# Kernel optimization log

Measured on AMD Instinct MI355X. Metric: run time of the kernel, lower is better.

Reference implementation:

```python
import jax, jax.numpy as jnp
import numpy as np

N = 100000      # nodes
E = 1600000     # edges (avg degree 16)
D_IN, D_H, D_OUT = 128, 128, 40
BN_EPS = 1e-5


def _gcn_norm(edge_index):
    # add self-loops, compute symmetric normalization D^-1/2 (A+I) D^-1/2
    loops = jnp.arange(N, dtype=edge_index.dtype)
    src = jnp.concatenate([edge_index[0], loops])
    dst = jnp.concatenate([edge_index[1], loops])
    deg = jax.ops.segment_sum(jnp.ones(src.shape[0], jnp.float32), dst, num_segments=N)
    dinv = jnp.where(deg > 0, jax.lax.rsqrt(deg), 0.0)
    norm = dinv[src] * dinv[dst]  # [E+N]
    return src, dst, norm


def _gcn_conv(h, W, b, src, dst, norm):
    h = h @ W                          # [N, d_out]
    msg = h[src] * norm[:, None]       # [E+N, d_out] gather + scale
    out = jax.ops.segment_sum(msg, dst, num_segments=N)
    return out + b


def _bn(h, g, beta, mean, var):
    return g * (h - mean) * jax.lax.rsqrt(var + BN_EPS) + beta


def setup_inputs() -> dict:
    key = jax.random.key(0)
    ks = jax.random.split(key, 16)
    x = jax.random.normal(ks[0], (N, D_IN), jnp.float32)
    edge_index = jax.random.randint(ks[1], (2, E), 0, N, dtype=jnp.int32)
    s_in, s_h = 1.0 / np.sqrt(D_IN), 1.0 / np.sqrt(D_H)
    W0 = jax.random.normal(ks[2], (D_IN, D_H), jnp.float32) * s_in
    b0 = jnp.zeros((D_H,), jnp.float32)
    W1 = jax.random.normal(ks[3], (D_H, D_H), jnp.float32) * s_h
    b1 = jnp.zeros((D_H,), jnp.float32)
    W2 = jax.random.normal(ks[4], (D_H, D_OUT), jnp.float32) * s_h
    b2 = jnp.zeros((D_OUT,), jnp.float32)
    g0 = jnp.ones((D_H,), jnp.float32)
    be0 = jnp.zeros((D_H,), jnp.float32)
    m0 = jax.random.normal(ks[5], (D_H,), jnp.float32) * 0.1
    v0 = jax.random.uniform(ks[6], (D_H,), jnp.float32) + 0.5
    g1 = jnp.ones((D_H,), jnp.float32)
    be1 = jnp.zeros((D_H,), jnp.float32)
    m1 = jax.random.normal(ks[7], (D_H,), jnp.float32) * 0.1
    v1 = jax.random.uniform(ks[8], (D_H,), jnp.float32) + 0.5
    return {"x": x, "edge_index": edge_index,
            "W0": W0, "b0": b0, "W1": W1, "b1": b1, "W2": W2, "b2": b2,
            "g0": g0, "be0": be0, "m0": m0, "v0": v0,
            "g1": g1, "be1": be1, "m1": m1, "v1": v1}


def reference(x, edge_index, W0, b0, W1, b1, W2, b2,
              g0, be0, m0, v0, g1, be1, m1, v1):
    src, dst, norm = _gcn_norm(edge_index)
    h = _gcn_conv(x, W0, b0, src, dst, norm)
    h = jax.nn.relu(_bn(h, g0, be0, m0, v0))   # dropout = identity in eval
    h = _gcn_conv(h, W1, b1, src, dst, norm)
    h = jax.nn.relu(_bn(h, g1, be1, m1, v1))
    h = _gcn_conv(h, W2, b2, src, dst, norm)
    return jax.nn.log_softmax(h, axis=1)
```

## Files before the change

### kernel.cpp

```cpp
#include <hip/hip_runtime.h>
#include <math.h>


#define CSHIFT 9
#define CSZ 512
#define PCHUNK 4096

typedef unsigned short u16;
typedef unsigned int u32;
typedef unsigned char u8;
typedef float f32x4 __attribute__((ext_vector_type(4)));
typedef short s16x8 __attribute__((ext_vector_type(8)));

__device__ inline float bflo(u32 u) { return __uint_as_float(u << 16); }
__device__ inline float bfhi(u32 u) { return __uint_as_float(u & 0xffff0000u); }
__device__ inline u16 f2bf(float f) {
    u32 b = __float_as_uint(f);
    b += 0x7fff + ((b >> 16) & 1);
    return (u16)(b >> 16);
}
__device__ inline u32 pack2(float lo, float hi) {
    return (u32)f2bf(lo) | ((u32)f2bf(hi) << 16);
}


__global__ __launch_bounds__(256) void k_hist1(const int* __restrict__ dst,
                                               int* __restrict__ hist1,
                                               int E, int NB) {
    __shared__ int h[256];
    int t = threadIdx.x;
    h[t] = 0;
    __syncthreads();
    for (int i = blockIdx.x * 256 * 16 + t; i < min(E, (blockIdx.x + 1) * 256 * 16);
         i += 256)
        atomicAdd(&h[dst[i] >> CSHIFT], 1);
    __syncthreads();
    if (t < NB && h[t]) atomicAdd(&hist1[t], h[t]);
}

__global__ __launch_bounds__(256) void k_scan1(const int* __restrict__ hist1,
                                               int* __restrict__ base1,
                                               int* __restrict__ cur1,
                                               int NB, int E) {
    __shared__ int sc[256];
    int t = threadIdx.x;
    int v = (t < NB) ? hist1[t] : 0;
    sc[t] = v;
    __syncthreads();
    for (int d = 1; d < 256; d <<= 1) {
        int add = (t >= d) ? sc[t - d] : 0;
        __syncthreads();
        sc[t] += add;
        __syncthreads();
    }
    if (t < NB) {
        int excl = sc[t] - v;
        base1[t] = excl;
        cur1[t] = excl;
    }
    if (t == 0) base1[NB] = E;
}

__global__ __launch_bounds__(256) void k_part1(const int* __restrict__ src,
                                               const int* __restrict__ dst,
                                               int* __restrict__ cur1,
                                               u32* __restrict__ bkt,
                                               int E, int NB) {
    __shared__ u32 stage[PCHUNK];
    __shared__ u8 sbin[PCHUNK];
    __shared__ int cnt[256];
    __shared__ int lbase[256];
    __shared__ int lcur[256];
    __shared__ int gb[256];
    int t = threadIdx.x;
    int base = blockIdx.x * PCHUNK;
    int n = min(PCHUNK, E - base);
    cnt[t] = 0;
    __syncthreads();
    for (int i = t; i < n; i += 256) atomicAdd(&cnt[dst[base + i] >> CSHIFT], 1);
    __syncthreads();
    int v = cnt[t];
    lbase[t] = v;
    __syncthreads();
    for (int d = 1; d < 256; d <<= 1) {
        int add = (t >= d) ? lbase[t - d] : 0;
        __syncthreads();
        lbase[t] += add;
        __syncthreads();
    }
    {
        int excl = lbase[t] - v;
        __syncthreads();
        lbase[t] = excl;
        lcur[t] = excl;
        if (t < NB && v) gb[t] = atomicAdd(&cur1[t], v);
    }
    __syncthreads();
    for (int i = t; i < n; i += 256) {
        int d = dst[base + i];
        int s = src[base + i];
        int bin = d >> CSHIFT;
        int p = atomicAdd(&lcur[bin], 1);
        stage[p] = ((u32)s << CSHIFT) | (u32)(d & (CSZ - 1));
        sbin[p] = (u8)bin;
    }
    __syncthreads();
    for (int k = t; k < n; k += 256) {
        int bin = sbin[k];
        bkt[gb[bin] + (k - lbase[bin])] = stage[k];
    }
}

__global__ __launch_bounds__(1024) void k_csr(const u32* __restrict__ bkt,
                                              const int* __restrict__ base1,
                                              int* __restrict__ col,
                                              int* __restrict__ row,
                                              float* __restrict__ dinv,
                                              int N, int E) {
    __shared__ int deg[CSZ];
    __shared__ int cur[CSZ];
    int b = blockIdx.x;
    int t = threadIdx.x;
    int start = base1[b];
    int end = base1[b + 1];
    if (t < CSZ) deg[t] = 0;
    __syncthreads();
    for (int i = start + t; i < end; i += 1024)
        atomicAdd(&deg[bkt[i] & (CSZ - 1)], 1);
    __syncthreads();
    int v = (t < CSZ) ? deg[t] : 0;
    if (t < CSZ) cur[t] = v;
    __syncthreads();
    for (int d = 1; d < CSZ; d <<= 1) {
        int add = (t < CSZ && t >= d) ? cur[t - d] : 0;
        __syncthreads();
        if (t < CSZ) cur[t] += add;
        __syncthreads();
    }
    if (t < CSZ) {
        int excl = cur[t] - v;
        int node = (b << CSHIFT) + t;
        if (node < N) {
            row[node] = start + excl;
            dinv[node] = rsqrtf((float)(v + 1));
        }
        cur[t] = excl;
    }
    __syncthreads();
    for (int i = start + t; i < end; i += 1024) {
        u32 e = bkt[i];
        int p = start + atomicAdd(&cur[e & (CSZ - 1)], 1);
        col[p] = (int)(e >> CSHIFT);
    }
    if (b == 0 && t == 0) row[N] = E;
}


__global__ __launch_bounds__(256) void k_packW(const float* __restrict__ W,
                                               u16* __restrict__ Wpk) {
    int g = blockIdx.x * 256 + threadIdx.x;
    int j = g & 7;
    int l = (g >> 3) & 63;
    int f = g >> 9;
    int ct = f & 7, ks = f >> 3;
    int krow = ks * 32 + ((l >> 4) << 3) + j;
    int wcol = ct * 16 + (l & 15);
    Wpk[g] = f2bf(W[krow * 128 + wcol]);
}

__global__ __launch_bounds__(256) void k_packW40(const float* __restrict__ W,
                                                 u16* __restrict__ Wpk) {
    int g = blockIdx.x * 256 + threadIdx.x;
    if (g >= 12 * 512) return;
    int j = g & 7;
    int l = (g >> 3) & 63;
    int f = g >> 9;
    int ct = f % 3, ks = f / 3;
    int krow = ks * 32 + ((l >> 4) << 3) + j;
    int wcol = ct * 16 + (l & 15);
    Wpk[g] = (wcol < 40) ? f2bf(W[krow * 40 + wcol]) : (u16)0;
}


__global__ __launch_bounds__(256) void k_gemm0(const float* __restrict__ A,
                                               const u16* __restrict__ Wpk,
                                               u16* __restrict__ C,
                                               const float* __restrict__ dinv,
                                               int M) {
    int tid = threadIdx.x;
    int wv = blockIdx.x * 4 + (tid >> 6);
    int rowbase = wv * 16;
    if (rowbase >= M) return;
    int l = tid & 63;
    int r = l & 15, hi = l >> 4;

    f32x4 acc[8];
#pragma unroll
    for (int ct = 0; ct < 8; ++ct) acc[ct] = (f32x4)(0.f);

    const uint4* wp = (const uint4*)Wpk;
#pragma unroll
    for (int ks = 0; ks < 4; ++ks) {
        int abase = (min(rowbase + r, M - 1)) * 128 + ks * 32 + hi * 8;
        float4 a0 = *(const float4*)&A[abase];
        float4 a1 = *(const float4*)&A[abase + 4];
        uint4 u = make_uint4(pack2(a0.x, a0.y), pack2(a0.z, a0.w),
                             pack2(a1.x, a1.y), pack2(a1.z, a1.w));
        s16x8 afrag = *(s16x8*)&u;
#pragma unroll
        for (int ct = 0; ct < 8; ++ct) {
            uint4 b = wp[(ks * 8 + ct) * 64 + l];
            s16x8 bfrag = *(s16x8*)&b;
            acc[ct] = __builtin_amdgcn_mfma_f32_16x16x32_bf16(afrag, bfrag, acc[ct], 0, 0, 0);
        }
    }
#pragma unroll
    for (int ct = 0; ct < 8; ++ct) {
#pragma unroll
        for (int reg = 0; reg < 4; ++reg) {
            int orow = rowbase + 4 * hi + reg;
            if (orow < M)
                C[(size_t)orow * 128 + ct * 16 + r] = f2bf(dinv[orow] * acc[ct][reg]);
        }
    }
}


template <int NCT>
__global__ __launch_bounds__(256) void k_fused(const u16* __restrict__ X,
                                               const u16* __restrict__ Wpk,
                                               u16* __restrict__ O,
                                               const int* __restrict__ row,
                                               const int* __restrict__ col,
                                               const float* __restrict__ dinv,
                                               const float* __restrict__ bias,
                                               const float* __restrict__ g,
                                               const float* __restrict__ be,
                                               const float* __restrict__ mean,
                                               const float* __restrict__ var,
                                               int n, int ostride) {
    __shared__ u32 hl[4][2][64];
    int tid = threadIdx.x;
    int wid = tid >> 6, lane = tid & 63;
    int half = lane >> 5, l5 = lane & 31;
    int node = (blockIdx.x * 4 + wid) * 2 + half;
    int nc = min(node, n - 1);
    const uint2* xp = (const uint2*)X;
    int s = row[nc], e = row[nc + 1];

    uint2 v = xp[(size_t)nc * 32 + l5];
    float a0 = bflo(v.x), a1 = bfhi(v.x), a2 = bflo(v.y), a3 = bfhi(v.y);
    float b0 = 0, b1 = 0, b2 = 0, b3 = 0;
    float c0 = 0, c1 = 0, c2 = 0, c3 = 0;
    float d0 = 0, d1 = 0, d2 = 0, d3 = 0;
    int j = s;
    for (; j + 8 <= e; j += 8) {
        int e0 = col[j], e1 = col[j+1], e2 = col[j+2], e3 = col[j+3];
        int e4 = col[j+4], e5 = col[j+5], e6 = col[j+6], e7 = col[j+7];
        uint2 x0 = xp[(size_t)e0 * 32 + l5];
        uint2 x1 = xp[(size_t)e1 * 32 + l5];
        uint2 x2 = xp[(size_t)e2 * 32 + l5];
        uint2 x3 = xp[(size_t)e3 * 32 + l5];
        uint2 x4 = xp[(size_t)e4 * 32 + l5];
        uint2 x5 = xp[(size_t)e5 * 32 + l5];
        uint2 x6 = xp[(size_t)e6 * 32 + l5];
        uint2 x7 = xp[(size_t)e7 * 32 + l5];
        a0 += bflo(x0.x); a1 += bfhi(x0.x); a2 += bflo(x0.y); a3 += bfhi(x0.y);
        b0 += bflo(x1.x); b1 += bfhi(x1.x); b2 += bflo(x1.y); b3 += bfhi(x1.y);
        c0 += bflo(x2.x); c1 += bfhi(x2.x); c2 += bflo(x2.y); c3 += bfhi(x2.y);
        d0 += bflo(x3.x); d1 += bfhi(x3.x); d2 += bflo(x3.y); d3 += bfhi(x3.y);
        a0 += bflo(x4.x); a1 += bfhi(x4.x); a2 += bflo(x4.y); a3 += bfhi(x4.y);
        b0 += bflo(x5.x); b1 += bfhi(x5.x); b2 += bflo(x5.y); b3 += bfhi(x5.y);
        c0 += bflo(x6.x); c1 += bfhi(x6.x); c2 += bflo(x6.y); c3 += bfhi(x6.y);
        d0 += bflo(x7.x); d1 += bfhi(x7.x); d2 += bflo(x7.y); d3 += bfhi(x7.y);
    }
    for (; j + 2 <= e; j += 2) {
        int e0 = col[j], e1 = col[j+1];
        uint2 x0 = xp[(size_t)e0 * 32 + l5];
        uint2 x1 = xp[(size_t)e1 * 32 + l5];
        a0 += bflo(x0.x); a1 += bfhi(x0.x); a2 += bflo(x0.y); a3 += bfhi(x0.y);
        b0 += bflo(x1.x); b1 += bfhi(x1.x); b2 += bflo(x1.y); b3 += bfhi(x1.y);
    }
    if (j < e) {
        uint2 x0 = xp[(size_t)col[j] * 32 + l5];
        c0 += bflo(x0.x); c1 += bfhi(x0.x); c2 += bflo(x0.y); c3 += bfhi(x0.y);
    }
    float dvn = dinv[nc];
    float s0 = dvn * ((a0 + b0) + (c0 + d0));
    float s1 = dvn * ((a1 + b1) + (c1 + d1));
    float s2 = dvn * ((a2 + b2) + (c2 + d2));
    float s3 = dvn * ((a3 + b3) + (c3 + d3));
    float4 g4 = ((const float4*)g)[l5];
    float4 be4 = ((const float4*)be)[l5];
    float4 m4 = ((const float4*)mean)[l5];
    float4 v4 = ((const float4*)var)[l5];
    float4 bi4 = ((const float4*)bias)[l5];
    float sc0 = g4.x * rsqrtf(v4.x + 1e-5f);
    float sc1 = g4.y * rsqrtf(v4.y + 1e-5f);
    float sc2 = g4.z * rsqrtf(v4.z + 1e-5f);
    float sc3 = g4.w * rsqrtf(v4.w + 1e-5f);
    float y0 = fmaxf(fmaf(sc0, s0, fmaf(sc0, bi4.x - m4.x, be4.x)), 0.f);
    float y1 = fmaxf(fmaf(sc1, s1, fmaf(sc1, bi4.y - m4.y, be4.y)), 0.f);
    float y2 = fmaxf(fmaf(sc2, s2, fmaf(sc2, bi4.z - m4.z, be4.z)), 0.f);
    float y3 = fmaxf(fmaf(sc3, s3, fmaf(sc3, bi4.w - m4.w, be4.w)), 0.f);

    *(uint2*)&hl[wid][half][l5 * 2] = make_uint2(pack2(y0, y1), pack2(y2, y3));

    int l = lane;
    int r1 = l & 1, hi = l >> 4;
    int node0 = (blockIdx.x * 4 + wid) * 2;
    int node1 = node0 + 1;
    float dv0 = dinv[min(node0, n - 1)];
    float dv1 = dinv[min(node1, n - 1)];
    const uint4* wp = (const uint4*)Wpk;
    const u32* hw = &hl[wid][0][0];
#pragma unroll
    for (int ct = 0; ct < NCT; ++ct) {
        f32x4 acc = (f32x4)(0.f);
#pragma unroll
        for (int ks = 0; ks < 4; ++ks) {
            uint4 a = *(const uint4*)&hw[r1 * 64 + ks * 16 + hi * 4];
            s16x8 afrag = *(s16x8*)&a;
            uint4 b = wp[(ks * NCT + ct) * 64 + l];
            s16x8 bfrag = *(s16x8*)&b;
            acc = __builtin_amdgcn_mfma_f32_16x16x32_bf16(afrag, bfrag, acc, 0, 0, 0);
        }
        if (l < 16) {
            int oc = ct * 16 + l;
            if (NCT == 8 || oc < 40) {
                if (node0 < n) O[(size_t)node0 * ostride + oc] = f2bf(dv0 * acc[0]);
                if (node1 < n) O[(size_t)node1 * ostride + oc] = f2bf(dv1 * acc[1]);
            }
        }
    }
}


__global__ __launch_bounds__(256) void k_agg40(const u16* __restrict__ X,
                                               float* __restrict__ out,
                                               const int* __restrict__ row,
                                               const int* __restrict__ col,
                                               const float* __restrict__ dinv,
                                               const float* __restrict__ b2,
                                               int n) {
    int tid = threadIdx.x;
    int wid = tid >> 6, lane = tid & 63;
    int half = lane >> 5, l5 = lane & 31;
    int node = (blockIdx.x * 4 + wid) * 2 + half;
    bool valid = node < n;
    int nc = valid ? node : (n - 1);
    bool active = l5 < 20;
    const u32* xp = (const u32*)X;
    int s = row[nc], e = row[nc + 1];
    int li = min(l5, 19);
    float a0 = 0, a1 = 0, b0 = 0, b1 = 0, c0 = 0, c1 = 0, d0 = 0, d1 = 0;
    {
        u32 v = xp[(size_t)nc * 20 + li];
        a0 = bflo(v); a1 = bfhi(v);
    }
    int j = s;
    for (; j + 8 <= e; j += 8) {
        int e0 = col[j], e1 = col[j+1], e2 = col[j+2], e3 = col[j+3];
        int e4 = col[j+4], e5 = col[j+5], e6 = col[j+6], e7 = col[j+7];
        u32 x0 = xp[(size_t)e0 * 20 + li];
        u32 x1 = xp[(size_t)e1 * 20 + li];
        u32 x2 = xp[(size_t)e2 * 20 + li];
        u32 x3 = xp[(size_t)e3 * 20 + li];
        u32 x4 = xp[(size_t)e4 * 20 + li];
        u32 x5 = xp[(size_t)e5 * 20 + li];
        u32 x6 = xp[(size_t)e6 * 20 + li];
        u32 x7 = xp[(size_t)e7 * 20 + li];
        a0 += bflo(x0); a1 += bfhi(x0);
        b0 += bflo(x1); b1 += bfhi(x1);
        c0 += bflo(x2); c1 += bfhi(x2);
        d0 += bflo(x3); d1 += bfhi(x3);
        a0 += bflo(x4); a1 += bfhi(x4);
        b0 += bflo(x5); b1 += bfhi(x5);
        c0 += bflo(x6); c1 += bfhi(x6);
        d0 += bflo(x7); d1 += bfhi(x7);
    }
    for (; j + 2 <= e; j += 2) {
        int e0 = col[j], e1 = col[j+1];
        u32 x0 = xp[(size_t)e0 * 20 + li];
        u32 x1 = xp[(size_t)e1 * 20 + li];
        a0 += bflo(x0); a1 += bfhi(x0);
        b0 += bflo(x1); b1 += bfhi(x1);
    }
    if (j < e) {
        u32 x0 = xp[(size_t)col[j] * 20 + li];
        c0 += bflo(x0); c1 += bfhi(x0);
    }
    float dv = dinv[nc];
    float ylo = -INFINITY, yhi = -INFINITY;
    if (active) {
        float2 bb = ((const float2*)b2)[l5];
        ylo = fmaf(dv, (a0 + b0) + (c0 + d0), bb.x);
        yhi = fmaf(dv, (a1 + b1) + (c1 + d1), bb.y);
    }
    float m = fmaxf(ylo, yhi);
#pragma unroll
    for (int d = 16; d; d >>= 1) m = fmaxf(m, __shfl_xor(m, d));
    float ex = active ? (__expf(ylo - m) + __expf(yhi - m)) : 0.f;
#pragma unroll
    for (int d = 16; d; d >>= 1) ex += __shfl_xor(ex, d);
    if (valid && active) {
        float lse = m + __logf(ex);
        ((float2*)out)[(size_t)node * 20 + l5] = make_float2(ylo - lse, yhi - lse);
    }
}


extern "C" void kernel_launch(void* const* d_in, const int* in_sizes, int n_in,
                              void* d_out, int out_size, void* d_ws, size_t ws_size,
                              hipStream_t stream) {
    const float* x   = (const float*)d_in[0];
    const int*   ei  = (const int*)d_in[1];
    const float* W0  = (const float*)d_in[2];
    const float* b0  = (const float*)d_in[3];
    const float* W1  = (const float*)d_in[4];
    const float* b1  = (const float*)d_in[5];
    const float* W2  = (const float*)d_in[6];
    const float* b2  = (const float*)d_in[7];
    const float* g0  = (const float*)d_in[8];
    const float* be0 = (const float*)d_in[9];
    const float* m0  = (const float*)d_in[10];
    const float* v0  = (const float*)d_in[11];
    const float* g1  = (const float*)d_in[12];
    const float* be1 = (const float*)d_in[13];
    const float* m1  = (const float*)d_in[14];
    const float* v1  = (const float*)d_in[15];
    float* out = (float*)d_out;

    int N = in_sizes[0] / 128;
    int E = in_sizes[1] / 2;
    const int* src = ei;
    const int* dst = ei + E;

    int NB = (N + CSZ - 1) / CSZ;

    char* ws = (char*)d_ws;
    size_t off = 0;
    auto alloc = [&](size_t bytes) -> char* {
        char* p = ws + off;
        off += (bytes + 255) & ~(size_t)255;
        return p;
    };
    u16*   XsA   = (u16*)alloc((size_t)N * 128 * 2);
    u16*   XsB   = (u16*)alloc((size_t)N * 128 * 2);
    u16*   bufC  = (u16*)alloc((size_t)N * 40 * 2);
    int*   col   = (int*)alloc((size_t)E * 4 + 64);
    int*   row   = (int*)alloc((size_t)(N + 1) * 4);
    float* dinv  = (float*)alloc((size_t)N * 4);
    int*   hist1 = (int*)alloc((size_t)(NB + 1) * 4);
    int*   base1 = (int*)alloc((size_t)(NB + 1) * 4);
    int*   cur1  = (int*)alloc((size_t)(NB + 1) * 4);
    u16*   Wpk0  = (u16*)alloc(128 * 128 * 2);
    u16*   Wpk1  = (u16*)alloc(128 * 128 * 2);
    u16*   Wpk2  = (u16*)alloc(128 * 48 * 2);
    u32*   bkt   = (u32*)XsA;

    hipMemsetAsync(hist1, 0, (size_t)(NB + 1) * 4, stream);
    k_hist1<<<(E + 4095) / 4096, 256, 0, stream>>>(dst, hist1, E, NB);
    k_scan1<<<1, 256, 0, stream>>>(hist1, base1, cur1, NB, E);
    k_part1<<<(E + PCHUNK - 1) / PCHUNK, 256, 0, stream>>>(src, dst, cur1, bkt, E, NB);
    k_csr<<<NB, 1024, 0, stream>>>(bkt, base1, col, row, dinv, N, E);
    k_packW<<<64, 256, 0, stream>>>(W0, Wpk0);
    k_packW<<<64, 256, 0, stream>>>(W1, Wpk1);
    k_packW40<<<24, 256, 0, stream>>>(W2, Wpk2);

    int gemmGrid = ((N + 15) / 16 + 3) / 4;
    k_gemm0<<<gemmGrid, 256, 0, stream>>>(x, Wpk0, XsA, dinv, N);
    int fusedGrid = (N + 7) / 8;
    k_fused<8><<<fusedGrid, 256, 0, stream>>>(XsA, Wpk1, XsB, row, col, dinv,
                                              b0, g0, be0, m0, v0, N, 128);
    k_fused<3><<<fusedGrid, 256, 0, stream>>>(XsB, Wpk2, bufC, row, col, dinv,
                                              b1, g1, be1, m1, v1, N, 40);
    k_agg40<<<(N + 7) / 8, 256, 0, stream>>>(bufC, out, row, col, dinv, b2, N);
}
```

Baseline: 311.2 us.

## Share block-wide MFMA across 8 nodes with XOR-swizzled LDS and split column tiles

The fused aggregate+transform kernel previously had each wave run a 16x16 MFMA on only its own 2 nodes, so most rows were wasted and every wave looped over all column tiles. Now all 8 nodes of the block are staged in a shared LDS tile behind a block barrier, and each wave computes a subset of column tiles for all 8 rows. The LDS layout uses an XOR swizzle to avoid bank conflicts. This cuts redundant MFMA and weight loads per node, at the cost of a __syncthreads, per-row dinv loads, and idle waves in the 40-column case.

```diff
diff --git a/kernel.cpp b/kernel.cpp
--- a/kernel.cpp
+++ b/kernel.cpp
@@ -239,11 +239,12 @@
                                                const float* __restrict__ mean,
                                                const float* __restrict__ var,
                                                int n, int ostride) {
-    __shared__ u32 hl[4][2][64];
+    __shared__ u32 hl[8][64];
     int tid = threadIdx.x;
     int wid = tid >> 6, lane = tid & 63;
     int half = lane >> 5, l5 = lane & 31;
-    int node = (blockIdx.x * 4 + wid) * 2 + half;
+    int nl = wid * 2 + half;
+    int node = blockIdx.x * 8 + nl;
     int nc = min(node, n - 1);
     const uint2* xp = (const uint2*)X;
     int s = row[nc], e = row[nc + 1];
@@ -303,33 +304,39 @@
     float y1 = fmaxf(fmaf(sc1, s1, fmaf(sc1, bi4.y - m4.y, be4.y)), 0.f);
     float y2 = fmaxf(fmaf(sc2, s2, fmaf(sc2, bi4.z - m4.z, be4.z)), 0.f);
     float y3 = fmaxf(fmaf(sc3, s3, fmaf(sc3, bi4.w - m4.w, be4.w)), 0.f);
-
-    *(uint2*)&hl[wid][half][l5 * 2] = make_uint2(pack2(y0, y1), pack2(y2, y3));
+    {
+        int unit = (l5 >> 1) ^ nl;
+        uint2* p = (uint2*)&hl[nl][(unit << 2) + ((l5 & 1) << 1)];
+        *p = make_uint2(pack2(y0, y1), pack2(y2, y3));
+    }
+    __syncthreads();
 
     int l = lane;
-    int r1 = l & 1, hi = l >> 4;
-    int node0 = (blockIdx.x * 4 + wid) * 2;
-    int node1 = node0 + 1;
-    float dv0 = dinv[min(node0, n - 1)];
-    float dv1 = dinv[min(node1, n - 1)];
+    int r = l & 15, hi = l >> 4;
+    int r7 = r & 7;
+    int nbase = blockIdx.x * 8;
     const uint4* wp = (const uint4*)Wpk;
-    const u32* hw = &hl[wid][0][0];
-#pragma unroll
-    for (int ct = 0; ct < NCT; ++ct) {
+    int ct0 = (NCT == 8) ? wid * 2 : wid;
+    int nct = (NCT == 8) ? 2 : (wid < 3 ? 1 : 0);
+    for (int ci = 0; ci < nct; ++ci) {
+        int ct = ct0 + ci;
         f32x4 acc = (f32x4)(0.f);
 #pragma unroll
         for (int ks = 0; ks < 4; ++ks) {
-            uint4 a = *(const uint4*)&hw[r1 * 64 + ks * 16 + hi * 4];
+            int unit = (ks * 4 + hi) ^ r7;
+            uint4 a = *(const uint4*)&hl[r7][unit << 2];
             s16x8 afrag = *(s16x8*)&a;
             uint4 b = wp[(ks * NCT + ct) * 64 + l];
             s16x8 bfrag = *(s16x8*)&b;
             acc = __builtin_amdgcn_mfma_f32_16x16x32_bf16(afrag, bfrag, acc, 0, 0, 0);
         }
-        if (l < 16) {
-            int oc = ct * 16 + l;
-            if (NCT == 8 || oc < 40) {
-                if (node0 < n) O[(size_t)node0 * ostride + oc] = f2bf(dv0 * acc[0]);
-                if (node1 < n) O[(size_t)node1 * ostride + oc] = f2bf(dv1 * acc[1]);
+        if (hi < 2) {
+#pragma unroll
+            for (int reg = 0; reg < 4; ++reg) {
+                int orow = nbase + 4 * hi + reg;
+                int oc = ct * 16 + r;
+                if (orow < n && (NCT == 8 || oc < 40))
+                    O[(size_t)orow * ostride + oc] = f2bf(dinv[orow] * acc[reg]);
             }
         }
     }
```

Measured after the change: 285.3 us. 1.09x faster.

## Split fused aggregate+GEMM kernels into separate aggregation and MFMA GEMM passes

Applied to the files above, without the earlier changes.

Replaces the fused aggregate-then-transform kernels with a standalone aggregation kernel (with BN and ReLU) that writes bf16 activations, followed by a generic templated MFMA GEMM kernel. The fused version did a small 2-row MFMA per wave, wasting most of each 16-row tile and staging through LDS. The split version uses full 16-row tiles but adds an extra global write and read of the N×128 intermediate for each layer, plus two more kernel launches.

```diff
diff --git a/kernel.cpp b/kernel.cpp
--- a/kernel.cpp
+++ b/kernel.cpp
@@ -156,37 +156,27 @@
 }
 
 
+template <int NCT, int C>
 __global__ __launch_bounds__(256) void k_packW(const float* __restrict__ W,
                                                u16* __restrict__ Wpk) {
     int g = blockIdx.x * 256 + threadIdx.x;
+    if (g >= NCT * 4 * 512) return;
     int j = g & 7;
     int l = (g >> 3) & 63;
     int f = g >> 9;
-    int ct = f & 7, ks = f >> 3;
+    int ct = f % NCT, ks = f / NCT;
     int krow = ks * 32 + ((l >> 4) << 3) + j;
     int wcol = ct * 16 + (l & 15);
-    Wpk[g] = f2bf(W[krow * 128 + wcol]);
-}
-
-__global__ __launch_bounds__(256) void k_packW40(const float* __restrict__ W,
-                                                 u16* __restrict__ Wpk) {
-    int g = blockIdx.x * 256 + threadIdx.x;
-    if (g >= 12 * 512) return;
-    int j = g & 7;
-    int l = (g >> 3) & 63;
-    int f = g >> 9;
-    int ct = f % 3, ks = f / 3;
-    int krow = ks * 32 + ((l >> 4) << 3) + j;
-    int wcol = ct * 16 + (l & 15);
-    Wpk[g] = (wcol < 40) ? f2bf(W[krow * 40 + wcol]) : (u16)0;
-}
-
-
-__global__ __launch_bounds__(256) void k_gemm0(const float* __restrict__ A,
+    Wpk[g] = (wcol < C) ? f2bf(W[krow * C + wcol]) : (u16)0;
+}
+
+
+template <bool AFP32, int NCT>
+__global__ __launch_bounds__(256) void k_gemmN(const void* __restrict__ Av,
                                                const u16* __restrict__ Wpk,
                                                u16* __restrict__ C,
                                                const float* __restrict__ dinv,
-                                               int M) {
+                                               int M, int ostride) {
     int tid = threadIdx.x;
     int wv = blockIdx.x * 4 + (tid >> 6);
     int rowbase = wv * 16;
@@ -194,60 +184,66 @@
     int l = tid & 63;
     int r = l & 15, hi = l >> 4;
 
-    f32x4 acc[8];
-#pragma unroll
-    for (int ct = 0; ct < 8; ++ct) acc[ct] = (f32x4)(0.f);
+    f32x4 acc[NCT];
+#pragma unroll
+    for (int ct = 0; ct < NCT; ++ct) acc[ct] = (f32x4)(0.f);
 
     const uint4* wp = (const uint4*)Wpk;
 #pragma unroll
     for (int ks = 0; ks < 4; ++ks) {
+        s16x8 afrag;
         int abase = (min(rowbase + r, M - 1)) * 128 + ks * 32 + hi * 8;
-        float4 a0 = *(const float4*)&A[abase];
-        float4 a1 = *(const float4*)&A[abase + 4];
-        uint4 u = make_uint4(pack2(a0.x, a0.y), pack2(a0.z, a0.w),
-                             pack2(a1.x, a1.y), pack2(a1.z, a1.w));
-        s16x8 afrag = *(s16x8*)&u;
-#pragma unroll
-        for (int ct = 0; ct < 8; ++ct) {
-            uint4 b = wp[(ks * 8 + ct) * 64 + l];
+        if (AFP32) {
+            const float* A = (const float*)Av;
+            float4 a0 = *(const float4*)&A[abase];
+            float4 a1 = *(const float4*)&A[abase + 4];
+            uint4 u = make_uint4(pack2(a0.x, a0.y), pack2(a0.z, a0.w),
+                                 pack2(a1.x, a1.y), pack2(a1.z, a1.w));
+            afrag = *(s16x8*)&u;
+        } else {
+            const u16* A = (const u16*)Av;
+            uint4 u = *(const uint4*)&A[abase];
+            afrag = *(s16x8*)&u;
+        }
+#pragma unroll
+        for (int ct = 0; ct < NCT; ++ct) {
+            uint4 b = wp[(ks * NCT + ct) * 64 + l];
             s16x8 bfrag = *(s16x8*)&b;
             acc[ct] = __builtin_amdgcn_mfma_f32_16x16x32_bf16(afrag, bfrag, acc[ct], 0, 0, 0);
         }
     }
 #pragma unroll
-    for (int ct = 0; ct < 8; ++ct) {
+    for (int ct = 0; ct < NCT; ++ct) {
 #pragma unroll
         for (int reg = 0; reg < 4; ++reg) {
             int orow = rowbase + 4 * hi + reg;
-            if (orow < M)
-                C[(size_t)orow * 128 + ct * 16 + r] = f2bf(dinv[orow] * acc[ct][reg]);
+            int oc = ct * 16 + r;
+            if (orow < M && oc < ostride)
+                C[(size_t)orow * ostride + oc] = f2bf(dinv[orow] * acc[ct][reg]);
         }
     }
 }
 
 
-template <int NCT>
-__global__ __launch_bounds__(256) void k_fused(const u16* __restrict__ X,
-                                               const u16* __restrict__ Wpk,
-                                               u16* __restrict__ O,
-                                               const int* __restrict__ row,
-                                               const int* __restrict__ col,
-                                               const float* __restrict__ dinv,
-                                               const float* __restrict__ bias,
-                                               const float* __restrict__ g,
-                                               const float* __restrict__ be,
-                                               const float* __restrict__ mean,
-                                               const float* __restrict__ var,
-                                               int n, int ostride) {
-    __shared__ u32 hl[4][2][64];
+__global__ __launch_bounds__(256) void k_agg128(const u16* __restrict__ X,
+                                                u16* __restrict__ Y,
+                                                const int* __restrict__ row,
+                                                const int* __restrict__ col,
+                                                const float* __restrict__ dinv,
+                                                const float* __restrict__ bias,
+                                                const float* __restrict__ g,
+                                                const float* __restrict__ be,
+                                                const float* __restrict__ mean,
+                                                const float* __restrict__ var,
+                                                int n) {
     int tid = threadIdx.x;
     int wid = tid >> 6, lane = tid & 63;
     int half = lane >> 5, l5 = lane & 31;
     int node = (blockIdx.x * 4 + wid) * 2 + half;
-    int nc = min(node, n - 1);
+    bool valid = node < n;
+    int nc = valid ? node : (n - 1);
     const uint2* xp = (const uint2*)X;
     int s = row[nc], e = row[nc + 1];
-
     uint2 v = xp[(size_t)nc * 32 + l5];
     float a0 = bflo(v.x), a1 = bfhi(v.x), a2 = bflo(v.y), a3 = bfhi(v.y);
     float b0 = 0, b1 = 0, b2 = 0, b3 = 0;
@@ -285,11 +281,11 @@
         uint2 x0 = xp[(size_t)col[j] * 32 + l5];
         c0 += bflo(x0.x); c1 += bfhi(x0.x); c2 += bflo(x0.y); c3 += bfhi(x0.y);
     }
-    float dvn = dinv[nc];
-    float s0 = dvn * ((a0 + b0) + (c0 + d0));
-    float s1 = dvn * ((a1 + b1) + (c1 + d1));
-    float s2 = dvn * ((a2 + b2) + (c2 + d2));
-    float s3 = dvn * ((a3 + b3) + (c3 + d3));
+    float dv = dinv[nc];
+    float s0 = dv * ((a0 + b0) + (c0 + d0));
+    float s1 = dv * ((a1 + b1) + (c1 + d1));
+    float s2 = dv * ((a2 + b2) + (c2 + d2));
+    float s3 = dv * ((a3 + b3) + (c3 + d3));
     float4 g4 = ((const float4*)g)[l5];
     float4 be4 = ((const float4*)be)[l5];
     float4 m4 = ((const float4*)mean)[l5];
@@ -303,38 +299,13 @@
     float y1 = fmaxf(fmaf(sc1, s1, fmaf(sc1, bi4.y - m4.y, be4.y)), 0.f);
     float y2 = fmaxf(fmaf(sc2, s2, fmaf(sc2, bi4.z - m4.z, be4.z)), 0.f);
     float y3 = fmaxf(fmaf(sc3, s3, fmaf(sc3, bi4.w - m4.w, be4.w)), 0.f);
-
-    *(uint2*)&hl[wid][half][l5 * 2] = make_uint2(pack2(y0, y1), pack2(y2, y3));
-
-    int l = lane;
-    int r1 = l & 1, hi = l >> 4;
-    int node0 = (blockIdx.x * 4 + wid) * 2;
-    int node1 = node0 + 1;
-    float dv0 = dinv[min(node0, n - 1)];
-    float dv1 = dinv[min(node1, n - 1)];
-    const uint4* wp = (const uint4*)Wpk;
-    const u32* hw = &hl[wid][0][0];
-#pragma unroll
-    for (int ct = 0; ct < NCT; ++ct) {
-        f32x4 acc = (f32x4)(0.f);
-#pragma unroll
-        for (int ks = 0; ks < 4; ++ks) {
-            uint4 a = *(const uint4*)&hw[r1 * 64 + ks * 16 + hi * 4];
-            s16x8 afrag = *(s16x8*)&a;
-            uint4 b = wp[(ks * NCT + ct) * 64 + l];
-            s16x8 bfrag = *(s16x8*)&b;
-            acc = __builtin_amdgcn_mfma_f32_16x16x32_bf16(afrag, bfrag, acc, 0, 0, 0);
-        }
-        if (l < 16) {
-            int oc = ct * 16 + l;
-            if (NCT == 8 || oc < 40) {
-                if (node0 < n) O[(size_t)node0 * ostride + oc] = f2bf(dv0 * acc[0]);
-                if (node1 < n) O[(size_t)node1 * ostride + oc] = f2bf(dv1 * acc[1]);
-            }
-        }
-    }
-}
-
+    if (valid) {
+        uint2 o;
+        o.x = pack2(y0, y1);
+        o.y = pack2(y2, y3);
+        ((uint2*)Y)[(size_t)node * 32 + l5] = o;
+    }
+}
 
 __global__ __launch_bounds__(256) void k_agg40(const u16* __restrict__ X,
                                                float* __restrict__ out,
@@ -464,16 +435,15 @@
     k_scan1<<<1, 256, 0, stream>>>(hist1, base1, cur1, NB, E);
     k_part1<<<(E + PCHUNK - 1) / PCHUNK, 256, 0, stream>>>(src, dst, cur1, bkt, E, NB);
     k_csr<<<NB, 1024, 0, stream>>>(bkt, base1, col, row, dinv, N, E);
-    k_packW<<<64, 256, 0, stream>>>(W0, Wpk0);
-    k_packW<<<64, 256, 0, stream>>>(W1, Wpk1);
-    k_packW40<<<24, 256, 0, stream>>>(W2, Wpk2);
+    k_packW<8, 128><<<64, 256, 0, stream>>>(W0, Wpk0);
+    k_packW<8, 128><<<64, 256, 0, stream>>>(W1, Wpk1);
+    k_packW<3, 40><<<24, 256, 0, stream>>>(W2, Wpk2);
 
     int gemmGrid = ((N + 15) / 16 + 3) / 4;
-    k_gemm0<<<gemmGrid, 256, 0, stream>>>(x, Wpk0, XsA, dinv, N);
-    int fusedGrid = (N + 7) / 8;
-    k_fused<8><<<fusedGrid, 256, 0, stream>>>(XsA, Wpk1, XsB, row, col, dinv,
-                                              b0, g0, be0, m0, v0, N, 128);
-    k_fused<3><<<fusedGrid, 256, 0, stream>>>(XsB, Wpk2, bufC, row, col, dinv,
-                                              b1, g1, be1, m1, v1, N, 40);
+    k_gemmN<true, 8><<<gemmGrid, 256, 0, stream>>>(x, Wpk0, XsA, dinv, N, 128);
+    k_agg128<<<(N + 7) / 8, 256, 0, stream>>>(XsA, XsB, row, col, dinv, b0, g0, be0, m0, v0, N);
+    k_gemmN<false, 8><<<gemmGrid, 256, 0, stream>>>(XsB, Wpk1, XsA, dinv, N, 128);
+    k_agg128<<<(N + 7) / 8, 256, 0, stream>>>(XsA, XsB, row, col, dinv, b1, g1, be1, m1, v1, N);
+    k_gemmN<false, 3><<<gemmGrid, 256, 0, stream>>>(XsB, Wpk2, bufC, dinv, N, 40);
     k_agg40<<<(N + 7) / 8, 256, 0, stream>>>(bufC, out, row, col, dinv, b2, N);
 }
```

Result: faster. 288.3 us (-7.3%).
